# Kernel tuning notes

Measured on AMD Instinct MI355X. Metric: run time of the kernel, lower is better.

Reference implementation:

```python
import jax, jax.numpy as jnp
import numpy as np
import math

IN_IMGSIZE = (64, 64)
KERNEL = (3, 3)
STRIDE = (1, 1)


def find_same_padding(in_size, k, s):
    out_size = math.ceil(in_size / s)
    return max((out_size - 1) * s + k - in_size, 0)


def setup_inputs() -> dict:
    key = jax.random.key(0)
    k1, k2 = jax.random.split(key)
    in_ch, out_ch = 128, 256
    B = 32
    X = jax.random.normal(k1, (B, in_ch, IN_IMGSIZE[0], IN_IMGSIZE[1]), dtype=jnp.float32)
    # He-uniform init as in the torch module
    variance = 2.0 / (KERNEL[0] * KERNEL[1] * in_ch)
    bound = math.sqrt(3.0 * variance)
    weights = jax.random.uniform(k2, (out_ch, in_ch, KERNEL[0], KERNEL[1]),
                                 minval=-bound, maxval=bound, dtype=jnp.float32)
    biases = jnp.zeros((out_ch,), dtype=jnp.float32)
    return {"X": X, "weights": weights, "biases": biases}


def reference(X, weights, biases):
    # 'same' padding amounts (height_pad == width_pad here, so torch's
    # F.pad dim-ordering quirk in the original is a no-op)
    hp = find_same_padding(IN_IMGSIZE[0], KERNEL[0], STRIDE[0])
    wp = find_same_padding(IN_IMGSIZE[1], KERNEL[1], STRIDE[1])
    # Replicate torch pad order: first pair of pad_tuple (height halves) pads width,
    # second pair (width halves) pads height. Identical when hp == wp.
    X_pad = jnp.pad(X, ((0, 0), (0, 0),
                        (wp // 2, wp - wp // 2),
                        (hp // 2, hp - hp // 2)))
    # Dense one-hot projector einsum in the original == standard conv2d.
    out = jax.lax.conv_general_dilated(
        X_pad, weights, window_strides=STRIDE, padding='VALID',
        dimension_numbers=('NCHW', 'OIHW', 'NCHW'))
    return out + biases[None, :, None, None]
```

## Files before the change

### kernel.cpp

```cpp
#include <hip/hip_runtime.h>

#define B_N  32
#define CI   128
#define CO   256
#define HH   64
#define WW   64
#define HP   66
#define WP   66
#define KTOT 1152
#define PIX  4096

#define XT_ELEMS ((size_t)B_N * HP * WP * CI)
#define XT_BYTES (XT_ELEMS * 2)
#define WT_ELEMS ((size_t)CO * KTOT)
#define WT_BYTES (WT_ELEMS * 2)
#define WS_NEEDED (XT_BYTES + WT_BYTES)

#define AS1 __attribute__((address_space(1)))
#define AS3 __attribute__((address_space(3)))

typedef __attribute__((ext_vector_type(8))) short bf16x8;
typedef __attribute__((ext_vector_type(4))) float f32x4;
typedef __attribute__((ext_vector_type(8))) unsigned short us8;

__device__ __forceinline__ unsigned short f2bf(float f) {
    unsigned int u = __builtin_bit_cast(unsigned int, f);
    u += 0x7fffu + ((u >> 16) & 1u);
    return (unsigned short)(u >> 16);
}

__device__ __forceinline__ void gload_lds16(const void* g, void* l) {
    __builtin_amdgcn_global_load_lds((const AS1 unsigned int*)g,
                                     (AS3 unsigned int*)l, 16, 0, 0);
}

__global__ void k_transpose(const float* __restrict__ X, unsigned short* __restrict__ Xt) {
    int bh   = blockIdx.x;
    int b    = bh >> 6, h = bh & 63;
    int wv   = threadIdx.x >> 6;
    int lane = threadIdx.x & 63;
    const float* src = X + (((size_t)(b * CI + wv * 32) * HH + h) << 6) + lane;
    us8 v[4];
#pragma unroll
    for (int j = 0; j < 32; ++j)
        v[j >> 3][j & 7] = f2bf(src[(size_t)j << 12]);
    unsigned short* dst = Xt + ((size_t)(b * HP + h + 1) * WP + (lane + 1)) * CI + wv * 32;
#pragma unroll
    for (int q = 0; q < 4; ++q)
        *(us8*)(dst + q * 8) = v[q];
}

__global__ void k_prepw(const float* __restrict__ W, unsigned short* __restrict__ Wt) {
    int co = blockIdx.x;
    for (int k = threadIdx.x; k < KTOT; k += 256) {
        int tap = k >> 7, ci = k & 127;
        Wt[(size_t)co * KTOT + k] = f2bf(W[((size_t)co * CI + ci) * 9 + tap]);
    }
}

__global__ __launch_bounds__(256, 2) void k_conv_gemm(
    const unsigned short* __restrict__ Xt, const unsigned short* __restrict__ Wt,
    const float* __restrict__ bias, float* __restrict__ out) {

    __shared__ __attribute__((aligned(16))) unsigned short As[128 * 64];
    __shared__ __attribute__((aligned(16))) unsigned short Bs[128 * 64];

    const int bid = blockIdx.x;
    const int b   = bid >> 6;
    const int mb  = (bid >> 5) & 1;
    const int nb  = bid & 31;
    const int co0 = mb << 7;
    const int h0  = nb << 1;

    const int tid  = threadIdx.x;
    const int wv   = tid >> 6;
    const int lane = tid & 63;
    const int lr   = lane & 15;
    const int lg   = lane >> 4;
    const int wm   = wv >> 1, wn = wv & 1;

    const int srow = lane >> 3;
    const int sg   = (lane & 7) ^ srow;

    f32x4 acc[4][4] = {};

    for (int s = 0; s < 18; ++s) {
        const int tap = s >> 1;
        const int ci0 = (s & 1) << 6;
        const int kh  = tap / 3;
        const int kw  = tap - kh * 3;
#pragma unroll
        for (int ii = 0; ii < 4; ++ii) {
            const int i = (wv << 2) + ii;
            const int arow = co0 + (i << 3) + srow;
            gload_lds16(Wt + (size_t)arow * KTOT + (s << 6) + (sg << 3), &As[i << 9]);
            const int pl = (i << 3) + srow;
            const int hh = h0 + (pl >> 6) + kh;
            const int wc = (pl & 63) + kw;
            gload_lds16(Xt + ((size_t)(b * HP + hh) * WP + wc) * CI + ci0 + (sg << 3),
                        &Bs[i << 9]);
        }
        __syncthreads();
#pragma unroll
        for (int kk = 0; kk < 2; ++kk) {
            bf16x8 af[4], bfr[4];
#pragma unroll
            for (int m = 0; m < 4; ++m) {
                const int row = (wm << 6) + (m << 4) + lr;
                const int g   = ((kk << 2) + lg) ^ (row & 7);
                af[m] = *(const bf16x8*)&As[(row << 6) + (g << 3)];
            }
#pragma unroll
            for (int n = 0; n < 4; ++n) {
                const int row = (wn << 6) + (n << 4) + lr;
                const int g   = ((kk << 2) + lg) ^ (row & 7);
                bfr[n] = *(const bf16x8*)&Bs[(row << 6) + (g << 3)];
            }
#pragma unroll
            for (int m = 0; m < 4; ++m)
#pragma unroll
                for (int n = 0; n < 4; ++n)
                    acc[m][n] = __builtin_amdgcn_mfma_f32_16x16x32_bf16(
                        af[m], bfr[n], acc[m][n], 0, 0, 0);
        }
        __syncthreads();
    }

    const int p0 = nb << 7;
#pragma unroll
    for (int m = 0; m < 4; ++m) {
#pragma unroll
        for (int j = 0; j < 4; ++j) {
            const int co = co0 + (wm << 6) + (m << 4) + (lg << 2) + j;
            const float bv = bias[co];
            float* op = out + ((size_t)(b * CO + co) << 12) + p0 + (wn << 6) + lr;
#pragma unroll
            for (int n = 0; n < 4; ++n)
                op[n << 4] = acc[m][n][j] + bv;
        }
    }
}

__global__ void k_naive(const float* __restrict__ X, const float* __restrict__ W,
                        const float* __restrict__ bias, float* __restrict__ out) {
    long idx = (long)blockIdx.x * blockDim.x + threadIdx.x;
    if (idx >= (long)B_N * CO * PIX) return;
    int p = idx & 4095, co = (int)((idx >> 12) & 255), b = (int)(idx >> 20);
    int h = p >> 6, w = p & 63;
    float s = bias[co];
    for (int ci = 0; ci < CI; ++ci) {
        const float* xp = X + ((size_t)(b * CI + ci) << 12);
        const float* wp = W + ((size_t)(co * CI + ci)) * 9;
        for (int kh = 0; kh < 3; ++kh) {
            int hh2 = h + kh - 1; if ((unsigned)hh2 >= 64u) continue;
            for (int kw = 0; kw < 3; ++kw) {
                int ww2 = w + kw - 1; if ((unsigned)ww2 >= 64u) continue;
                s += xp[(hh2 << 6) + ww2] * wp[kh * 3 + kw];
            }
        }
    }
    out[idx] = s;
}

extern "C" void kernel_launch(void* const* d_in, const int* in_sizes, int n_in,
                              void* d_out, int out_size, void* d_ws, size_t ws_size,
                              hipStream_t stream) {
    const float* X    = (const float*)d_in[0];
    const float* W    = (const float*)d_in[1];
    const float* bias = (const float*)d_in[2];
    float* out = (float*)d_out;

    if (ws_size < WS_NEEDED) {
        long total = (long)B_N * CO * PIX;
        k_naive<<<(int)((total + 255) / 256), 256, 0, stream>>>(X, W, bias, out);
        return;
    }

    unsigned short* Xt = (unsigned short*)d_ws;
    unsigned short* Wt = (unsigned short*)((char*)d_ws + XT_BYTES);

    hipMemsetAsync(d_ws, 0, XT_BYTES, stream);
    k_transpose<<<B_N * HH, 256, 0, stream>>>(X, Xt);
    k_prepw<<<CO, 256, 0, stream>>>(W, Wt);
    k_conv_gemm<<<B_N * 64, 256, 0, stream>>>(Xt, Wt, bias, out);
}
```

Baseline: 116.8 us.

## Use 256x256 double-buffered conv GEMM tiles and zero padding borders in transpose

The GEMM tile grows from 128x128 per 256-thread block to 256x256 per 512-thread block. LDS is now double-buffered, and the loads for the next K-step are interleaved with MFMA quadrants under fine-grained vmcnt waits and barriers, with setprio raised around the MFMAs. Block IDs are remapped to group work across XCDs, and the full-buffer memset is replaced by zeroing only the halo rows and columns inside the transpose kernel. This is meant to hide global-load latency and cut memset traffic, at the cost of 128KB LDS per block (which may limit occupancy to one block per CU) and a more fragile schedule.

Measured after the change: 119.0 us. Within noise of the previous version (+1.9%).

```diff
diff --git a/kernel.cpp b/kernel.cpp
--- a/kernel.cpp
+++ b/kernel.cpp
@@ -19,22 +19,23 @@
 #define AS1 __attribute__((address_space(1)))
 #define AS3 __attribute__((address_space(3)))
 
+typedef unsigned short us;
 typedef __attribute__((ext_vector_type(8))) short bf16x8;
 typedef __attribute__((ext_vector_type(4))) float f32x4;
 typedef __attribute__((ext_vector_type(8))) unsigned short us8;
 
-__device__ __forceinline__ unsigned short f2bf(float f) {
+__device__ __forceinline__ us f2bf(float f) {
     unsigned int u = __builtin_bit_cast(unsigned int, f);
     u += 0x7fffu + ((u >> 16) & 1u);
-    return (unsigned short)(u >> 16);
-}
-
-__device__ __forceinline__ void gload_lds16(const void* g, void* l) {
+    return (us)(u >> 16);
+}
+
+__device__ __forceinline__ void gload16(const void* g, const void* l) {
     __builtin_amdgcn_global_load_lds((const AS1 unsigned int*)g,
                                      (AS3 unsigned int*)l, 16, 0, 0);
 }
 
-__global__ void k_transpose(const float* __restrict__ X, unsigned short* __restrict__ Xt) {
+__global__ void k_transpose(const float* __restrict__ X, us* __restrict__ Xt) {
     int bh   = blockIdx.x;
     int b    = bh >> 6, h = bh & 63;
     int wv   = threadIdx.x >> 6;
@@ -44,13 +45,28 @@
 #pragma unroll
     for (int j = 0; j < 32; ++j)
         v[j >> 3][j & 7] = f2bf(src[(size_t)j << 12]);
-    unsigned short* dst = Xt + ((size_t)(b * HP + h + 1) * WP + (lane + 1)) * CI + wv * 32;
+    us* dst = Xt + ((size_t)(b * HP + h + 1) * WP + (lane + 1)) * CI + wv * 32;
 #pragma unroll
     for (int q = 0; q < 4; ++q)
         *(us8*)(dst + q * 8) = v[q];
-}
-
-__global__ void k_prepw(const float* __restrict__ W, unsigned short* __restrict__ Wt) {
+    us8 z = (us8)0;
+    int t = threadIdx.x;
+    if (t < 32) {
+        int wcol = (t < 16) ? 0 : 65;
+        int i = t & 15;
+        *(us8*)(Xt + ((size_t)(b * HP + h + 1) * WP + wcol) * CI + i * 8) = z;
+    }
+    if (h == 0) {
+        for (int i = t; i < WP * CI / 8; i += 256)
+            *(us8*)(Xt + (size_t)(b * HP + 0) * WP * CI + (size_t)i * 8) = z;
+    }
+    if (h == 63) {
+        for (int i = t; i < WP * CI / 8; i += 256)
+            *(us8*)(Xt + (size_t)(b * HP + 65) * WP * CI + (size_t)i * 8) = z;
+    }
+}
+
+__global__ void k_prepw(const float* __restrict__ W, us* __restrict__ Wt) {
     int co = blockIdx.x;
     for (int k = threadIdx.x; k < KTOT; k += 256) {
         int tap = k >> 7, ci = k & 127;
@@ -58,85 +74,130 @@
     }
 }
 
-__global__ __launch_bounds__(256, 2) void k_conv_gemm(
-    const unsigned short* __restrict__ Xt, const unsigned short* __restrict__ Wt,
+__global__ __launch_bounds__(512, 2) void k_conv_gemm(
+    const us* __restrict__ Xt, const us* __restrict__ Wt,
     const float* __restrict__ bias, float* __restrict__ out) {
 
-    __shared__ __attribute__((aligned(16))) unsigned short As[128 * 64];
-    __shared__ __attribute__((aligned(16))) unsigned short Bs[128 * 64];
-
-    const int bid = blockIdx.x;
-    const int b   = bid >> 6;
-    const int mb  = (bid >> 5) & 1;
-    const int nb  = bid & 31;
-    const int co0 = mb << 7;
-    const int h0  = nb << 1;
+    __shared__ __attribute__((aligned(16))) us As[2][256 * 64];
+    __shared__ __attribute__((aligned(16))) us Bs[2][256 * 64];
+
+    const int bid0 = blockIdx.x;
+    const int bid  = (bid0 & 7) * 64 + (bid0 >> 3);
+    const int b    = bid >> 4;
+    const int nb   = bid & 15;
+    const int h0   = nb << 2;
 
     const int tid  = threadIdx.x;
+    const int lane = tid & 63;
     const int wv   = tid >> 6;
-    const int lane = tid & 63;
-    const int lr   = lane & 15;
-    const int lg   = lane >> 4;
-    const int wm   = wv >> 1, wn = wv & 1;
-
-    const int srow = lane >> 3;
-    const int sg   = (lane & 7) ^ srow;
-
-    f32x4 acc[4][4] = {};
-
-    for (int s = 0; s < 18; ++s) {
-        const int tap = s >> 1;
-        const int ci0 = (s & 1) << 6;
-        const int kh  = tap / 3;
-        const int kw  = tap - kh * 3;
-#pragma unroll
-        for (int ii = 0; ii < 4; ++ii) {
-            const int i = (wv << 2) + ii;
-            const int arow = co0 + (i << 3) + srow;
-            gload_lds16(Wt + (size_t)arow * KTOT + (s << 6) + (sg << 3), &As[i << 9]);
-            const int pl = (i << 3) + srow;
-            const int hh = h0 + (pl >> 6) + kh;
-            const int wc = (pl & 63) + kw;
-            gload_lds16(Xt + ((size_t)(b * HP + hh) * WP + wc) * CI + ci0 + (sg << 3),
-                        &Bs[i << 9]);
-        }
-        __syncthreads();
-#pragma unroll
-        for (int kk = 0; kk < 2; ++kk) {
-            bf16x8 af[4], bfr[4];
-#pragma unroll
-            for (int m = 0; m < 4; ++m) {
-                const int row = (wm << 6) + (m << 4) + lr;
-                const int g   = ((kk << 2) + lg) ^ (row & 7);
-                af[m] = *(const bf16x8*)&As[(row << 6) + (g << 3)];
-            }
-#pragma unroll
-            for (int n = 0; n < 4; ++n) {
-                const int row = (wn << 6) + (n << 4) + lr;
-                const int g   = ((kk << 2) + lg) ^ (row & 7);
-                bfr[n] = *(const bf16x8*)&Bs[(row << 6) + (g << 3)];
-            }
+    const int lr   = lane & 15, lg = lane >> 4;
+    const int wm   = wv >> 2,  wn = wv & 3;
+
+    const int srow = tid >> 3;
+    const int sg   = (tid & 7) ^ (srow & 7);
+
+    f32x4 acc[8][4] = {};
+
+    auto stageA = [&](int slot, int t, int qm) {
+#pragma unroll
+        for (int c = 0; c < 2; ++c) {
+            const int r0 = qm * 64 + c * 128;
+            const us* src = Wt + (size_t)(r0 + srow) * KTOT + t * 64 + sg * 8;
+            const us* d   = &As[slot][(r0 + (wv << 3)) * 64];
+            gload16(src, d);
+        }
+    };
+    auto stageB = [&](int slot, int t, int qn) {
+        const int tap = t >> 1, ci0 = (t & 1) << 6;
+        const int kh = tap / 3, kw = tap - kh * 3;
+#pragma unroll
+        for (int c = 0; c < 2; ++c) {
+            const int r  = qn * 128 + c * 64 + srow;
+            const int p  = ((r >> 5) & 3) * 64 + (r >> 7) * 32 + (r & 31);
+            const int hh = h0 + (p >> 6) + kh;
+            const int wc = (p & 63) + kw;
+            const us* src = Xt + ((size_t)(b * HP + hh) * WP + wc) * CI + ci0 + sg * 8;
+            const us* d   = &Bs[slot][(qn * 128 + c * 64 + (wv << 3)) * 64];
+            gload16(src, d);
+        }
+    };
+
+    bf16x8 a[4][2], bb[2][2];
+    auto ldA = [&](int slot, int qm) {
+#pragma unroll
+        for (int m = 0; m < 4; ++m)
+#pragma unroll
+            for (int kk = 0; kk < 2; ++kk) {
+                const int row = wm * 128 + qm * 64 + m * 16 + lr;
+                const int g   = (kk * 4 + lg) ^ (row & 7);
+                a[m][kk] = *(const bf16x8*)&As[slot][row * 64 + g * 8];
+            }
+    };
+    auto ldB = [&](int slot, int qn) {
+#pragma unroll
+        for (int n = 0; n < 2; ++n)
+#pragma unroll
+            for (int kk = 0; kk < 2; ++kk) {
+                const int r = qn * 128 + wn * 32 + n * 16 + lr;
+                const int g = (kk * 4 + lg) ^ (r & 7);
+                bb[n][kk] = *(const bf16x8*)&Bs[slot][r * 64 + g * 8];
+            }
+    };
+    auto mma = [&](int qm, int qn) {
+        __builtin_amdgcn_s_setprio(1);
+#pragma unroll
+        for (int kk = 0; kk < 2; ++kk)
 #pragma unroll
             for (int m = 0; m < 4; ++m)
 #pragma unroll
-                for (int n = 0; n < 4; ++n)
-                    acc[m][n] = __builtin_amdgcn_mfma_f32_16x16x32_bf16(
-                        af[m], bfr[n], acc[m][n], 0, 0, 0);
-        }
-        __syncthreads();
-    }
-
-    const int p0 = nb << 7;
-#pragma unroll
-    for (int m = 0; m < 4; ++m) {
+                for (int n = 0; n < 2; ++n)
+                    acc[qm * 4 + m][qn * 2 + n] = __builtin_amdgcn_mfma_f32_16x16x32_bf16(
+                        a[m][kk], bb[n][kk], acc[qm * 4 + m][qn * 2 + n], 0, 0, 0);
+        __builtin_amdgcn_s_setprio(0);
+    };
+
+    stageA(0, 0, 0);
+    stageB(0, 0, 0);
+    stageA(0, 0, 1);
+    stageB(0, 0, 1);
+
+    for (int t = 0; t < 18; ++t) {
+        const int s = t & 1, ns = s ^ 1;
+        const int tn = (t < 17) ? t + 1 : 17;
+        asm volatile("s_waitcnt vmcnt(4)" ::: "memory");
+        __builtin_amdgcn_s_barrier();
+        stageA(ns, tn, 0);
+        ldA(s, 0); ldB(s, 0);
+        mma(0, 0);
+        asm volatile("s_waitcnt vmcnt(4)" ::: "memory");
+        __builtin_amdgcn_s_barrier();
+        stageB(ns, tn, 0);
+        ldA(s, 1);
+        mma(1, 0);
+        asm volatile("s_waitcnt vmcnt(4)" ::: "memory");
+        __builtin_amdgcn_s_barrier();
+        stageA(ns, tn, 1);
+        ldB(s, 1);
+        mma(1, 1);
+        stageB(ns, tn, 1);
+        ldA(s, 0);
+        mma(0, 1);
+    }
+
+    const int p0base = nb * 256 + wn * 64;
+#pragma unroll
+    for (int mf = 0; mf < 8; ++mf) {
+        const int qm = mf >> 2, m = mf & 3;
 #pragma unroll
         for (int j = 0; j < 4; ++j) {
-            const int co = co0 + (wm << 6) + (m << 4) + (lg << 2) + j;
+            const int co = wm * 128 + qm * 64 + m * 16 + lg * 4 + j;
             const float bv = bias[co];
-            float* op = out + ((size_t)(b * CO + co) << 12) + p0 + (wn << 6) + lr;
-#pragma unroll
-            for (int n = 0; n < 4; ++n)
-                op[n << 4] = acc[m][n][j] + bv;
+            float* op = out + ((size_t)(b * CO + co) << 12) + p0base + lr;
+#pragma unroll
+            for (int nf = 0; nf < 4; ++nf) {
+                const int qn = nf >> 1, n = nf & 1;
+                op[qn * 32 + n * 16] = acc[mf][nf][j] + bv;
+            }
         }
     }
 }
@@ -176,11 +237,10 @@
         return;
     }
 
-    unsigned short* Xt = (unsigned short*)d_ws;
-    unsigned short* Wt = (unsigned short*)((char*)d_ws + XT_BYTES);
-
-    hipMemsetAsync(d_ws, 0, XT_BYTES, stream);
+    us* Xt = (us*)d_ws;
+    us* Wt = (us*)((char*)d_ws + XT_BYTES);
+
     k_transpose<<<B_N * HH, 256, 0, stream>>>(X, Xt);
     k_prepw<<<CO, 256, 0, stream>>>(W, Wt);
-    k_conv_gemm<<<B_N * 64, 256, 0, stream>>>(Xt, Wt, bias, out);
-}
+    k_conv_gemm<<<512, 512, 0, stream>>>(Xt, Wt, bias, out);
+}
```

## Use 32x32x16 MFMA tiles and zero padding borders inside transpose kernel

Applied to the files above, without the earlier changes.

The GEMM inner loop switches from 16x16x32 to 32x32x16 bf16 MFMA, with a 2x2 grid of 32x32 accumulators per wave. This halves the number of LDS fragment reads per MFMA and changes the epilogue row mapping to match. The full-workspace memset is removed; the transpose kernel now zeroes only the padding columns and the top and bottom padding rows. This avoids writing the whole padded buffer twice, at the cost of extra branches in the transpose.

After: 113.1 us. 1.03x faster.

```diff
diff --git a/kernel.cpp b/kernel.cpp
--- a/kernel.cpp
+++ b/kernel.cpp
@@ -3,8 +3,6 @@
 #define B_N  32
 #define CI   128
 #define CO   256
-#define HH   64
-#define WW   64
 #define HP   66
 #define WP   66
 #define KTOT 1152
@@ -12,45 +10,58 @@
 
 #define XT_ELEMS ((size_t)B_N * HP * WP * CI)
 #define XT_BYTES (XT_ELEMS * 2)
-#define WT_ELEMS ((size_t)CO * KTOT)
-#define WT_BYTES (WT_ELEMS * 2)
+#define WT_BYTES ((size_t)CO * KTOT * 2)
 #define WS_NEEDED (XT_BYTES + WT_BYTES)
 
 #define AS1 __attribute__((address_space(1)))
 #define AS3 __attribute__((address_space(3)))
 
+typedef unsigned short us;
 typedef __attribute__((ext_vector_type(8))) short bf16x8;
-typedef __attribute__((ext_vector_type(4))) float f32x4;
+typedef __attribute__((ext_vector_type(16))) float f32x16;
 typedef __attribute__((ext_vector_type(8))) unsigned short us8;
 
-__device__ __forceinline__ unsigned short f2bf(float f) {
+__device__ __forceinline__ us f2bf(float f) {
     unsigned int u = __builtin_bit_cast(unsigned int, f);
     u += 0x7fffu + ((u >> 16) & 1u);
-    return (unsigned short)(u >> 16);
+    return (us)(u >> 16);
 }
 
-__device__ __forceinline__ void gload_lds16(const void* g, void* l) {
+__device__ __forceinline__ void gload16(const void* g, const void* l) {
     __builtin_amdgcn_global_load_lds((const AS1 unsigned int*)g,
                                      (AS3 unsigned int*)l, 16, 0, 0);
 }
 
-__global__ void k_transpose(const float* __restrict__ X, unsigned short* __restrict__ Xt) {
+__global__ void k_transpose(const float* __restrict__ X, us* __restrict__ Xt) {
     int bh   = blockIdx.x;
     int b    = bh >> 6, h = bh & 63;
     int wv   = threadIdx.x >> 6;
     int lane = threadIdx.x & 63;
-    const float* src = X + (((size_t)(b * CI + wv * 32) * HH + h) << 6) + lane;
+    const float* src = X + (((size_t)(b * CI + wv * 32) * 64 + h) << 6) + lane;
     us8 v[4];
 #pragma unroll
     for (int j = 0; j < 32; ++j)
         v[j >> 3][j & 7] = f2bf(src[(size_t)j << 12]);
-    unsigned short* dst = Xt + ((size_t)(b * HP + h + 1) * WP + (lane + 1)) * CI + wv * 32;
+    us* dst = Xt + ((size_t)(b * HP + h + 1) * WP + (lane + 1)) * CI + wv * 32;
 #pragma unroll
     for (int q = 0; q < 4; ++q)
         *(us8*)(dst + q * 8) = v[q];
+    us8 z = (us8)0;
+    int t = threadIdx.x;
+    if (t < 32) {
+        int wcol = (t < 16) ? 0 : 65;
+        int i = t & 15;
+        *(us8*)(Xt + ((size_t)(b * HP + h + 1) * WP + wcol) * CI + i * 8) = z;
+    }
+    if (h == 0)
+        for (int i = t; i < WP * CI / 8; i += 256)
+            *(us8*)(Xt + (size_t)(b * HP + 0) * WP * CI + (size_t)i * 8) = z;
+    if (h == 63)
+        for (int i = t; i < WP * CI / 8; i += 256)
+            *(us8*)(Xt + (size_t)(b * HP + 65) * WP * CI + (size_t)i * 8) = z;
 }
 
-__global__ void k_prepw(const float* __restrict__ W, unsigned short* __restrict__ Wt) {
+__global__ void k_prepw(const float* __restrict__ W, us* __restrict__ Wt) {
     int co = blockIdx.x;
     for (int k = threadIdx.x; k < KTOT; k += 256) {
         int tap = k >> 7, ci = k & 127;
@@ -59,11 +70,11 @@
 }
 
 __global__ __launch_bounds__(256, 2) void k_conv_gemm(
-    const unsigned short* __restrict__ Xt, const unsigned short* __restrict__ Wt,
+    const us* __restrict__ Xt, const us* __restrict__ Wt,
     const float* __restrict__ bias, float* __restrict__ out) {
 
-    __shared__ __attribute__((aligned(16))) unsigned short As[128 * 64];
-    __shared__ __attribute__((aligned(16))) unsigned short Bs[128 * 64];
+    __shared__ __attribute__((aligned(16))) us As[128 * 64];
+    __shared__ __attribute__((aligned(16))) us Bs[128 * 64];
 
     const int bid = blockIdx.x;
     const int b   = bid >> 6;
@@ -75,14 +86,14 @@
     const int tid  = threadIdx.x;
     const int wv   = tid >> 6;
     const int lane = tid & 63;
-    const int lr   = lane & 15;
-    const int lg   = lane >> 4;
+    const int l31  = lane & 31;
+    const int hi   = lane >> 5;
     const int wm   = wv >> 1, wn = wv & 1;
 
     const int srow = lane >> 3;
     const int sg   = (lane & 7) ^ srow;
 
-    f32x4 acc[4][4] = {};
+    f32x16 acc[2][2] = {};
 
     for (int s = 0; s < 18; ++s) {
         const int tap = s >> 1;
@@ -93,50 +104,50 @@
         for (int ii = 0; ii < 4; ++ii) {
             const int i = (wv << 2) + ii;
             const int arow = co0 + (i << 3) + srow;
-            gload_lds16(Wt + (size_t)arow * KTOT + (s << 6) + (sg << 3), &As[i << 9]);
+            gload16(Wt + (size_t)arow * KTOT + (s << 6) + (sg << 3), &As[i << 9]);
             const int pl = (i << 3) + srow;
             const int hh = h0 + (pl >> 6) + kh;
             const int wc = (pl & 63) + kw;
-            gload_lds16(Xt + ((size_t)(b * HP + hh) * WP + wc) * CI + ci0 + (sg << 3),
-                        &Bs[i << 9]);
+            gload16(Xt + ((size_t)(b * HP + hh) * WP + wc) * CI + ci0 + (sg << 3),
+                    &Bs[i << 9]);
         }
         __syncthreads();
 #pragma unroll
-        for (int kk = 0; kk < 2; ++kk) {
-            bf16x8 af[4], bfr[4];
+        for (int ks = 0; ks < 4; ++ks) {
+            bf16x8 af[2], bfv[2];
 #pragma unroll
-            for (int m = 0; m < 4; ++m) {
-                const int row = (wm << 6) + (m << 4) + lr;
-                const int g   = ((kk << 2) + lg) ^ (row & 7);
+            for (int m = 0; m < 2; ++m) {
+                const int row = (wm << 6) + (m << 5) + l31;
+                const int g   = ((ks << 1) + hi) ^ (row & 7);
                 af[m] = *(const bf16x8*)&As[(row << 6) + (g << 3)];
             }
 #pragma unroll
-            for (int n = 0; n < 4; ++n) {
-                const int row = (wn << 6) + (n << 4) + lr;
-                const int g   = ((kk << 2) + lg) ^ (row & 7);
-                bfr[n] = *(const bf16x8*)&Bs[(row << 6) + (g << 3)];
+            for (int n = 0; n < 2; ++n) {
+                const int prow = (wn << 6) + (n << 5) + l31;
+                const int g    = ((ks << 1) + hi) ^ (prow & 7);
+                bfv[n] = *(const bf16x8*)&Bs[(prow << 6) + (g << 3)];
             }
 #pragma unroll
-            for (int m = 0; m < 4; ++m)
+            for (int m = 0; m < 2; ++m)
 #pragma unroll
-                for (int n = 0; n < 4; ++n)
-                    acc[m][n] = __builtin_amdgcn_mfma_f32_16x16x32_bf16(
-                        af[m], bfr[n], acc[m][n], 0, 0, 0);
+                for (int n = 0; n < 2; ++n)
+                    acc[m][n] = __builtin_amdgcn_mfma_f32_32x32x16_bf16(
+                        af[m], bfv[n], acc[m][n], 0, 0, 0);
         }
         __syncthreads();
     }
 
-    const int p0 = nb << 7;
+    const int p0 = (nb << 7) + (wn << 6);
 #pragma unroll
-    for (int m = 0; m < 4; ++m) {
+    for (int m = 0; m < 2; ++m) {
 #pragma unroll
-        for (int j = 0; j < 4; ++j) {
-            const int co = co0 + (wm << 6) + (m << 4) + (lg << 2) + j;
+        for (int j = 0; j < 16; ++j) {
+            const int co = co0 + (wm << 6) + (m << 5) + (j & 3) + ((j >> 2) << 3) + (hi << 2);
             const float bv = bias[co];
-            float* op = out + ((size_t)(b * CO + co) << 12) + p0 + (wn << 6) + lr;
+            float* op = out + ((size_t)(b * CO + co) << 12) + p0 + l31;
 #pragma unroll
-            for (int n = 0; n < 4; ++n)
-                op[n << 4] = acc[m][n][j] + bv;
+            for (int n = 0; n < 2; ++n)
+                op[n << 5] = acc[m][n][j] + bv;
         }
     }
 }
@@ -176,11 +187,10 @@
         return;
     }
 
-    unsigned short* Xt = (unsigned short*)d_ws;
-    unsigned short* Wt = (unsigned short*)((char*)d_ws + XT_BYTES);
+    us* Xt = (us*)d_ws;
+    us* Wt = (us*)((char*)d_ws + XT_BYTES);
 
-    hipMemsetAsync(d_ws, 0, XT_BYTES, stream);
-    k_transpose<<<B_N * HH, 256, 0, stream>>>(X, Xt);
+    k_transpose<<<B_N * 64, 256, 0, stream>>>(X, Xt);
     k_prepw<<<CO, 256, 0, stream>>>(W, Wt);
     k_conv_gemm<<<B_N * 64, 256, 0, stream>>>(Xt, Wt, bias, out);
 }
```
